# Performance work log

Measured on AMD Instinct MI355X. Metric: run time of the kernel, lower is better.

## Reference

```python
import jax, jax.numpy as jnp
import numpy as np

B, S, DM = 2, 2048, 1024
H, HD = 16, 64  # heads, head_dims = dims // heads
SCALE = HD ** -0.5


def softmax_one(x):
    # softmax with +1 in the denominator: exp(x_i) / (1 + sum_j exp(x_j))
    # stable form: shift by m = max(max(x), 0)
    m = jnp.maximum(jnp.max(x, axis=-1, keepdims=True), 0.0)
    e = jnp.exp(x - m)
    return e / (jnp.exp(-m) + jnp.sum(e, axis=-1, keepdims=True))


def setup_inputs() -> dict:
    key = jax.random.key(0)
    ks = jax.random.split(key, 11)
    init = lambda k, shape, fan_in: jax.random.uniform(k, shape, jnp.float32, -1.0, 1.0) * (fan_in ** -0.5)
    return {
        "query": jax.random.normal(ks[0], (B, S, DM), jnp.float32),
        "key": jax.random.normal(ks[1], (B, S, DM), jnp.float32),
        "value": jax.random.normal(ks[2], (B, S, DM), jnp.float32),
        "Wq": init(ks[3], (H * HD, DM), DM), "bq": init(ks[4], (H * HD,), DM),
        "Wk": init(ks[5], (H * HD, DM), DM), "bk": init(ks[6], (H * HD,), DM),
        "Wv": init(ks[7], (H * HD, DM), DM), "bv": init(ks[8], (H * HD,), DM),
        "Wo": init(ks[9], (DM, H * HD), H * HD), "bo": init(ks[10], (DM,), H * HD),
    }


def _proj(x, W, b):
    # [B,S,DM] -> [B,H,S,HD]
    y = x @ W.T + b
    return y.reshape(B, S, H, HD).transpose(0, 2, 1, 3)


def reference(query, key, value, Wq, bq, Wk, bk, Wv, bv, Wo, bo):
    Q = _proj(query, Wq, bq)
    K = _proj(key, Wk, bk)
    V = _proj(value, Wv, bv)
    scores = jnp.einsum("bhqd,bhkd->bhqk", Q, K) * SCALE  # [B,H,S,S]
    attn = softmax_one(scores)
    out = jnp.einsum("bhqk,bhkd->bhqd", attn, V)  # [B,H,S,HD]
    out = out.transpose(0, 2, 1, 3).reshape(B, S, H * HD)
    return out @ Wo.T + bo
```

## Files before the change

### kernel.cpp

```cpp
#include <hip/hip_runtime.h>

#define B_ 2
#define S_ 2048
#define DM_ 1024
#define H_ 16
#define HD_ 64
#define QSCALE_ 0.18033688011112042f

typedef __bf16 bf16;
typedef __attribute__((ext_vector_type(4))) __bf16 bf16x4;
typedef __attribute__((ext_vector_type(8))) __bf16 bf16x8;
typedef __attribute__((ext_vector_type(4))) float f32x4;

#define MFMA16(a, b, c) __builtin_amdgcn_mfma_f32_16x16x32_bf16((a), (b), (c), 0, 0, 0)
#define EXP2(x) __builtin_amdgcn_exp2f(x)

__device__ __forceinline__ void async16(const bf16* g, bf16* l) {
  __builtin_amdgcn_global_load_lds(
      (const __attribute__((address_space(1))) void*)g,
      (__attribute__((address_space(3))) void*)l, 16, 0, 0);
}

__global__ __launch_bounds__(256) void convert_kernel(
    const float* __restrict__ q, const float* __restrict__ k,
    const float* __restrict__ v, const float* __restrict__ wq,
    const float* __restrict__ wk, const float* __restrict__ wv,
    const float* __restrict__ wo, bf16* __restrict__ dst) {
  size_t idx = ((size_t)blockIdx.x * 256 + threadIdx.x) * 8;
  const float* src;
  size_t off;
  if (idx < 4194304) { src = q; off = idx; }
  else if (idx < 8388608) { src = k; off = idx - 4194304; }
  else if (idx < 12582912) { src = v; off = idx - 8388608; }
  else if (idx < 13631488) { src = wq; off = idx - 12582912; }
  else if (idx < 14680064) { src = wk; off = idx - 13631488; }
  else if (idx < 15728640) { src = wv; off = idx - 14680064; }
  else { src = wo; off = idx - 15728640; }
  float4 a = *(const float4*)(src + off);
  float4 b = *(const float4*)(src + off + 4);
  bf16x8 o;
  o[0] = (bf16)a.x; o[1] = (bf16)a.y; o[2] = (bf16)a.z; o[3] = (bf16)a.w;
  o[4] = (bf16)b.x; o[5] = (bf16)b.y; o[6] = (bf16)b.z; o[7] = (bf16)b.w;
  *(bf16x8*)(dst + idx) = o;
}

template <int MODE>
__device__ __forceinline__ void gemm_body(bf16* smem, const bf16* A,
                                          const bf16* W, const float* bias,
                                          bf16* C, float scale, int m0,
                                          int n0) {
  constexpr int K = 1024;
  bf16* As = smem;
  bf16* Bs = smem + 128 * 64;
  const int t = threadIdx.x;
  const int lane = t & 63, wave = t >> 6;
  const int quad = lane >> 4, l16 = lane & 15;
  const int wm = (wave >> 1) * 64, wn = (wave & 1) * 64;

  const f32x4 zero = {0.f, 0.f, 0.f, 0.f};
  f32x4 acc[4][4];
  for (int i = 0; i < 4; i++)
    for (int j = 0; j < 4; j++) acc[i][j] = zero;

  for (int k0 = 0; k0 < K; k0 += 64) {
    for (int i = 0; i < 4; ++i) {
      int c = i * 256 + t;
      int row = c >> 3, g = c & 7;
      int off = k0 + ((g ^ (row & 7)) * 8);
      async16(A + (size_t)(m0 + row) * K + off, As + c * 8);
      async16(W + (size_t)(n0 + row) * K + off, Bs + c * 8);
    }
    __syncthreads();

    for (int ks = 0; ks < 2; ks++) {
      bf16x8 af[4], bfr[4];
      for (int mb = 0; mb < 4; mb++) {
        int ra = wm + mb * 16 + l16;
        af[mb] = *(const bf16x8*)(As + ra * 64 + ((ks * 4 + quad) ^ (ra & 7)) * 8);
        int rb = wn + mb * 16 + l16;
        bfr[mb] = *(const bf16x8*)(Bs + rb * 64 + ((ks * 4 + quad) ^ (rb & 7)) * 8);
      }
      for (int mb = 0; mb < 4; mb++)
        for (int nb = 0; nb < 4; nb++)
          acc[mb][nb] = MFMA16(af[mb], bfr[nb], acc[mb][nb]);
    }
    __syncthreads();
  }

  if constexpr (MODE == 2) {
    bf16* Ct = smem;
    for (int nb = 0; nb < 4; nb++) {
      int cl = wn + nb * 16 + l16;
      float bv = bias[n0 + cl] * scale;
      for (int mb = 0; mb < 4; mb++) {
        int rowb = wm + mb * 16 + quad * 4;
        bf16x4 v;
        for (int r = 0; r < 4; r++)
          v[r] = (bf16)(acc[mb][nb][r] * scale + bv);
        *(bf16x4*)(Ct + cl * 136 + rowb) = v;
      }
    }
    __syncthreads();
    int c = t >> 1, half = t & 1;
    int colg = n0 + c;
    int hh = colg >> 6, dd = colg & 63;
    int bb = m0 >> 11, s0 = m0 & (S_ - 1);
    bf16* dst = C + (((size_t)(bb * H_ + hh)) * HD_ + dd) * S_ + s0 + half * 64;
    const bf16* srcr = Ct + c * 136 + half * 64;
    for (int j = 0; j < 8; ++j)
      *(bf16x8*)(dst + j * 8) = *(const bf16x8*)(srcr + j * 8);
  } else {
    for (int nb = 0; nb < 4; nb++) {
      int col = n0 + wn + nb * 16 + l16;
      float bv = bias[col] * scale;
      for (int mb = 0; mb < 4; mb++) {
        int rowb = m0 + wm + mb * 16 + quad * 4;
        for (int r = 0; r < 4; r++) {
          int row = rowb + r;
          float o = acc[mb][nb][r] * scale + bv;
          int bb = row >> 11, s = row & (S_ - 1);
          int h = col >> 6, d = col & 63;
          C[(((size_t)(bb * H_ + h)) * S_ + s) * HD_ + d] = (bf16)o;
        }
      }
    }
  }
}

__global__ __launch_bounds__(256, 4) void qkv_proj_kernel(
    const bf16* Xc, const float* bq, const float* bk, const float* bv,
    bf16* Qo, bf16* Ko, bf16* Vo) {
  __shared__ __align__(16) bf16 smem[128 * 136];
  int bid = blockIdx.x;
  int z = bid >> 8;
  int r = bid & 255;
  int c = r & 7;
  int j = r >> 3;
  int m0 = (c * 4 + (j & 3)) * 128;
  int n0 = (j >> 2) * 128;
  const bf16* A = Xc + (size_t)z * 4194304;
  const bf16* W = Xc + 12582912 + (size_t)z * 1048576;
  if (z == 0)
    gemm_body<1>(smem, A, W, bq, Qo, QSCALE_, m0, n0);
  else if (z == 1)
    gemm_body<1>(smem, A, W, bk, Ko, 1.0f, m0, n0);
  else
    gemm_body<2>(smem, A, W, bv, Vo, 1.0f, m0, n0);
}

__global__ __launch_bounds__(256, 4) void out_proj_kernel(const bf16* A,
                                                          const bf16* W,
                                                          const float* bias,
                                                          float* C) {
  constexpr int K = 1024, N = 1024;
  __shared__ __align__(16) bf16 As[64 * 64];
  __shared__ __align__(16) bf16 Bs[64 * 64];
  const int t = threadIdx.x;
  const int lane = t & 63, wave = t >> 6;
  const int quad = lane >> 4, l16 = lane & 15;
  int bid = blockIdx.x;
  int c = bid & 7;
  int j = bid >> 3;
  const int m0 = (c * 8 + (j & 7)) * 64;
  const int n0 = (j >> 3) * 64;

  const f32x4 zero = {0.f, 0.f, 0.f, 0.f};
  f32x4 acc[4];
  for (int i = 0; i < 4; i++) acc[i] = zero;

  for (int k0 = 0; k0 < K; k0 += 64) {
    for (int i = 0; i < 2; ++i) {
      int cc = i * 256 + t;
      int row = cc >> 3, g = cc & 7;
      int off = k0 + ((g ^ (row & 7)) * 8);
      async16(A + (size_t)(m0 + row) * K + off, As + cc * 8);
      async16(W + (size_t)(n0 + row) * K + off, Bs + cc * 8);
    }
    __syncthreads();

    for (int ks = 0; ks < 2; ks++) {
      int ra = wave * 16 + l16;
      bf16x8 af = *(const bf16x8*)(As + ra * 64 + ((ks * 4 + quad) ^ (ra & 7)) * 8);
      for (int nb = 0; nb < 4; nb++) {
        int rb = nb * 16 + l16;
        bf16x8 bfr =
            *(const bf16x8*)(Bs + rb * 64 + ((ks * 4 + quad) ^ (rb & 7)) * 8);
        acc[nb] = MFMA16(af, bfr, acc[nb]);
      }
    }
    __syncthreads();
  }

  for (int nb = 0; nb < 4; nb++) {
    int col = n0 + nb * 16 + l16;
    float bv = bias[col];
    int rowb = m0 + wave * 16 + quad * 4;
    for (int r = 0; r < 4; r++)
      C[(size_t)(rowb + r) * N + col] = acc[nb][r] + bv;
  }
}

__global__ __launch_bounds__(256, 2) void attn_kernel(
    const bf16* __restrict__ Q, const bf16* __restrict__ Kg,
    const bf16* __restrict__ VTg, bf16* __restrict__ O) {
  __shared__ __align__(16) bf16 Ks[128 * 64];
  __shared__ __align__(16) bf16 Vt[64 * 128];
  __shared__ __align__(16) bf16 Ps[4 * 64 * 72];
  __shared__ float rsL[2][64];
  const int t = threadIdx.x;
  const int lane = t & 63, wave = t >> 6;
  const int quad = lane >> 4, l16 = lane & 15;
  const int id = blockIdx.x;
  const int bh = id & 31;
  const int qt = id >> 5;
  const int q0 = qt * 128;
  const int b = bh >> 4, h = bh & 15;
  const int qhalf = wave >> 1, khalf = wave & 1;
  const size_t base = ((size_t)(b * H_ + h)) * S_ * HD_;
  const bf16* Qp = Q + base;
  const bf16* Kp = Kg + base;
  const bf16* Vp = VTg + base;

  bf16x8 aq[4][2];
  for (int s = 0; s < 4; s++) {
    const bf16* qr = Qp + (size_t)(q0 + qhalf * 64 + s * 16 + l16) * HD_;
    aq[s][0] = *(const bf16x8*)(qr + quad * 8);
    aq[s][1] = *(const bf16x8*)(qr + 32 + quad * 8);
  }

  const f32x4 zero = {0.f, 0.f, 0.f, 0.f};
  f32x4 oc[4][4];
  for (int s = 0; s < 4; s++)
    for (int d = 0; d < 4; d++) oc[s][d] = zero;
  float rs[4] = {0.f, 0.f, 0.f, 0.f};

  bf16* Pw = Ps + wave * (64 * 72);

  for (int kv0 = 0; kv0 < S_; kv0 += 128) {
    for (int i = 0; i < 4; ++i) {
      int c = i * 256 + t;
      int row = c >> 3, g = c & 7;
      async16(Kp + (size_t)(kv0 + row) * HD_ + (g ^ (row & 7)) * 8, Ks + c * 8);
    }
    for (int i = 0; i < 4; ++i) {
      int c = i * 256 + t;
      int d = c >> 4, g = c & 15;
      async16(Vp + (size_t)d * S_ + kv0 + (g ^ (d & 15)) * 8, Vt + c * 8);
    }
    __syncthreads();

    f32x4 sc[4][4];
    for (int s = 0; s < 4; s++)
      for (int nb = 0; nb < 4; nb++) sc[s][nb] = zero;
    for (int ks = 0; ks < 2; ks++) {
      for (int nb = 0; nb < 4; nb++) {
        int row = khalf * 64 + nb * 16 + l16;
        int slot = (ks * 4 + quad) ^ (row & 7);
        bf16x8 kf = *(const bf16x8*)(Ks + row * 64 + slot * 8);
        for (int s = 0; s < 4; s++)
          sc[s][nb] = MFMA16(kf, aq[s][ks], sc[s][nb]);
      }
    }

    for (int s = 0; s < 4; s++) {
      bf16* prow = Pw + (s * 16 + l16) * 72 + quad * 4;
      for (int nb = 0; nb < 4; nb++) {
        float p0 = EXP2(sc[s][nb][0]);
        float p1 = EXP2(sc[s][nb][1]);
        float p2 = EXP2(sc[s][nb][2]);
        float p3 = EXP2(sc[s][nb][3]);
        rs[s] += (p0 + p1) + (p2 + p3);
        bf16x4 pv = {(bf16)p0, (bf16)p1, (bf16)p2, (bf16)p3};
        *(bf16x4*)(prow + nb * 16) = pv;
      }
    }

    for (int ks2 = 0; ks2 < 2; ks2++) {
      bf16x8 vf[4];
      for (int db = 0; db < 4; db++) {
        int row = db * 16 + l16;
        int g = khalf * 8 + ks2 * 4 + quad;
        vf[db] = *(const bf16x8*)(Vt + row * 128 + (g ^ (row & 15)) * 8);
      }
      for (int s = 0; s < 4; s++) {
        bf16x8 ap =
            *(const bf16x8*)(Pw + (s * 16 + l16) * 72 + ks2 * 32 + quad * 8);
        for (int db = 0; db < 4; db++)
          oc[s][db] = MFMA16(ap, vf[db], oc[s][db]);
      }
    }
    __syncthreads();
  }

  float* Ld = (float*)Ps;
  if (khalf) {
    for (int s = 0; s < 4; s++) {
      float rtot = rs[s];
      rtot += __shfl_xor(rtot, 16);
      rtot += __shfl_xor(rtot, 32);
      if (quad == 0) rsL[qhalf][s * 16 + l16] = rtot;
      for (int db = 0; db < 4; db++)
        for (int r = 0; r < 4; r++)
          Ld[(size_t)qhalf * (64 * 68) + (s * 16 + quad * 4 + r) * 68 +
             db * 16 + l16] = oc[s][db][r];
    }
  }
  __syncthreads();
  if (!khalf) {
    for (int s = 0; s < 4; s++) {
      float rtot = rs[s];
      rtot += __shfl_xor(rtot, 16);
      rtot += __shfl_xor(rtot, 32);
      float l_all = 1.f + rtot + rsL[qhalf][s * 16 + l16];
      for (int r = 0; r < 4; r++) {
        float inv = 1.f / __shfl(l_all, quad * 4 + r);
        int qrow = q0 + qhalf * 64 + s * 16 + quad * 4 + r;
        size_t orow = ((size_t)(b * S_ + qrow) * H_ + h) * HD_;
        for (int db = 0; db < 4; db++) {
          float val = oc[s][db][r] +
                      Ld[(size_t)qhalf * (64 * 68) +
                         (s * 16 + quad * 4 + r) * 68 + db * 16 + l16];
          O[orow + db * 16 + l16] = (bf16)(val * inv);
        }
      }
    }
  }
}

extern "C" void kernel_launch(void* const* d_in, const int* in_sizes, int n_in,
                              void* d_out, int out_size, void* d_ws,
                              size_t ws_size, hipStream_t stream) {
  const float* query = (const float*)d_in[0];
  const float* key = (const float*)d_in[1];
  const float* value = (const float*)d_in[2];
  const float* bq = (const float*)d_in[4];
  const float* bk = (const float*)d_in[6];
  const float* bv = (const float*)d_in[8];
  const float* bo = (const float*)d_in[10];
  float* out = (float*)d_out;

  bf16* Xc = (bf16*)d_ws;
  bf16* Qw = Xc + 16777216;
  const size_t SZ = (size_t)B_ * H_ * S_ * HD_;
  bf16* Kw = Qw + SZ;
  bf16* Vw = Kw + SZ;
  bf16* Ow = Vw + SZ;

  convert_kernel<<<8192, 256, 0, stream>>>(query, key, value,
                                           (const float*)d_in[3],
                                           (const float*)d_in[5],
                                           (const float*)d_in[7],
                                           (const float*)d_in[9], Xc);
  qkv_proj_kernel<<<768, 256, 0, stream>>>(Xc, bq, bk, bv, Qw, Kw, Vw);
  attn_kernel<<<512, 256, 0, stream>>>(Qw, Kw, Vw, Ow);
  out_proj_kernel<<<1024, 256, 0, stream>>>(Ow, Xc + 15728640, bo, out);
}
```

Baseline: 206.1 us.

## Split attention KV tile across four waves with 64-row query tiles

The attention kernel now uses 512-thread blocks over 64-query tiles, so there are 1024 blocks instead of 512. Each of the 8 waves handles 32 query rows and one quarter of the 128-key tile, and the partial outputs and row sums are combined through a two-step LDS reduction. The goal is more parallelism and occupancy, with fewer registers per wave, to fill the GPU better. In exchange, each K/V tile is reloaded by twice as many blocks, per-wave MFMA work shrinks, and the epilogue adds an extra reduction pass and barrier.

After: 221.8 us. 7.6% more time.

```diff
diff --git a/kernel.cpp b/kernel.cpp
--- a/kernel.cpp
+++ b/kernel.cpp
@@ -200,71 +200,72 @@
   }
 }
 
-__global__ __launch_bounds__(256, 2) void attn_kernel(
+__global__ __launch_bounds__(512, 4) void attn_kernel(
     const bf16* __restrict__ Q, const bf16* __restrict__ Kg,
     const bf16* __restrict__ VTg, bf16* __restrict__ O) {
-  __shared__ __align__(16) bf16 Ks[128 * 64];
-  __shared__ __align__(16) bf16 Vt[64 * 128];
-  __shared__ __align__(16) bf16 Ps[4 * 64 * 72];
-  __shared__ float rsL[2][64];
+  __shared__ __align__(16) bf16 smem[26624];
   const int t = threadIdx.x;
   const int lane = t & 63, wave = t >> 6;
   const int quad = lane >> 4, l16 = lane & 15;
+  const int qh = wave >> 2;
+  const int kq = wave & 3;
   const int id = blockIdx.x;
   const int bh = id & 31;
   const int qt = id >> 5;
-  const int q0 = qt * 128;
+  const int q0 = qt * 64;
   const int b = bh >> 4, h = bh & 15;
-  const int qhalf = wave >> 1, khalf = wave & 1;
   const size_t base = ((size_t)(b * H_ + h)) * S_ * HD_;
   const bf16* Qp = Q + base;
   const bf16* Kp = Kg + base;
   const bf16* Vp = VTg + base;
 
-  bf16x8 aq[4][2];
-  for (int s = 0; s < 4; s++) {
-    const bf16* qr = Qp + (size_t)(q0 + qhalf * 64 + s * 16 + l16) * HD_;
+  bf16* Ks = smem;
+  bf16* Vt = smem + 8192;
+  bf16* Pw = smem + 16384 + wave * (32 * 40);
+
+  bf16x8 aq[2][2];
+  for (int s = 0; s < 2; s++) {
+    const bf16* qr = Qp + (size_t)(q0 + qh * 32 + s * 16 + l16) * HD_;
     aq[s][0] = *(const bf16x8*)(qr + quad * 8);
     aq[s][1] = *(const bf16x8*)(qr + 32 + quad * 8);
   }
 
   const f32x4 zero = {0.f, 0.f, 0.f, 0.f};
-  f32x4 oc[4][4];
-  for (int s = 0; s < 4; s++)
+  f32x4 oc[2][4];
+  for (int s = 0; s < 2; s++)
     for (int d = 0; d < 4; d++) oc[s][d] = zero;
-  float rs[4] = {0.f, 0.f, 0.f, 0.f};
-
-  bf16* Pw = Ps + wave * (64 * 72);
+  float rs[2] = {0.f, 0.f};
 
   for (int kv0 = 0; kv0 < S_; kv0 += 128) {
-    for (int i = 0; i < 4; ++i) {
-      int c = i * 256 + t;
-      int row = c >> 3, g = c & 7;
-      async16(Kp + (size_t)(kv0 + row) * HD_ + (g ^ (row & 7)) * 8, Ks + c * 8);
-    }
-    for (int i = 0; i < 4; ++i) {
-      int c = i * 256 + t;
-      int d = c >> 4, g = c & 15;
-      async16(Vp + (size_t)d * S_ + kv0 + (g ^ (d & 15)) * 8, Vt + c * 8);
-    }
-    __syncthreads();
-
-    f32x4 sc[4][4];
-    for (int s = 0; s < 4; s++)
-      for (int nb = 0; nb < 4; nb++) sc[s][nb] = zero;
+    for (int i = 0; i < 2; ++i) {
+      int cc = i * 512 + t;
+      int row = cc >> 3, g = cc & 7;
+      async16(Kp + (size_t)(kv0 + row) * HD_ + (g ^ (row & 7)) * 8,
+              Ks + cc * 8);
+    }
+    for (int i = 0; i < 2; ++i) {
+      int cc = i * 512 + t;
+      int d = cc >> 4, g = cc & 15;
+      async16(Vp + (size_t)d * S_ + kv0 + (g ^ (d & 15)) * 8, Vt + cc * 8);
+    }
+    __syncthreads();
+
+    f32x4 sc[2][2];
+    for (int s = 0; s < 2; s++)
+      for (int nb = 0; nb < 2; nb++) sc[s][nb] = zero;
     for (int ks = 0; ks < 2; ks++) {
-      for (int nb = 0; nb < 4; nb++) {
-        int row = khalf * 64 + nb * 16 + l16;
+      for (int nb = 0; nb < 2; nb++) {
+        int row = kq * 32 + nb * 16 + l16;
         int slot = (ks * 4 + quad) ^ (row & 7);
         bf16x8 kf = *(const bf16x8*)(Ks + row * 64 + slot * 8);
-        for (int s = 0; s < 4; s++)
+        for (int s = 0; s < 2; s++)
           sc[s][nb] = MFMA16(kf, aq[s][ks], sc[s][nb]);
       }
     }
 
-    for (int s = 0; s < 4; s++) {
-      bf16* prow = Pw + (s * 16 + l16) * 72 + quad * 4;
-      for (int nb = 0; nb < 4; nb++) {
+    for (int s = 0; s < 2; s++) {
+      bf16* prow = Pw + (s * 16 + l16) * 40 + quad * 4;
+      for (int nb = 0; nb < 2; nb++) {
         float p0 = EXP2(sc[s][nb][0]);
         float p1 = EXP2(sc[s][nb][1]);
         float p2 = EXP2(sc[s][nb][2]);
@@ -275,51 +276,72 @@
       }
     }
 
-    for (int ks2 = 0; ks2 < 2; ks2++) {
-      bf16x8 vf[4];
-      for (int db = 0; db < 4; db++) {
-        int row = db * 16 + l16;
-        int g = khalf * 8 + ks2 * 4 + quad;
-        vf[db] = *(const bf16x8*)(Vt + row * 128 + (g ^ (row & 15)) * 8);
-      }
-      for (int s = 0; s < 4; s++) {
-        bf16x8 ap =
-            *(const bf16x8*)(Pw + (s * 16 + l16) * 72 + ks2 * 32 + quad * 8);
-        for (int db = 0; db < 4; db++)
-          oc[s][db] = MFMA16(ap, vf[db], oc[s][db]);
-      }
-    }
-    __syncthreads();
-  }
-
-  float* Ld = (float*)Ps;
-  if (khalf) {
-    for (int s = 0; s < 4; s++) {
-      float rtot = rs[s];
-      rtot += __shfl_xor(rtot, 16);
-      rtot += __shfl_xor(rtot, 32);
-      if (quad == 0) rsL[qhalf][s * 16 + l16] = rtot;
+    bf16x8 vf[4];
+    for (int db = 0; db < 4; db++) {
+      int row = db * 16 + l16;
+      int g = kq * 4 + quad;
+      vf[db] = *(const bf16x8*)(Vt + row * 128 + (g ^ (row & 15)) * 8);
+    }
+    for (int s = 0; s < 2; s++) {
+      bf16x8 ap = *(const bf16x8*)(Pw + (s * 16 + l16) * 40 + quad * 8);
+      for (int db = 0; db < 4; db++)
+        oc[s][db] = MFMA16(ap, vf[db], oc[s][db]);
+    }
+
+    __syncthreads();
+  }
+
+  float rtot[2];
+  for (int s = 0; s < 2; s++) {
+    float v = rs[s];
+    v += __shfl_xor(v, 16);
+    v += __shfl_xor(v, 32);
+    rtot[s] = v;
+  }
+
+  float* Ld = (float*)smem;
+  float* rsL = (float*)(smem + 17408);
+
+  if (kq & 1) {
+    float* Lw = Ld + (size_t)((qh * 2 + (kq >> 1)) * 32) * 68;
+    for (int s = 0; s < 2; s++) {
       for (int db = 0; db < 4; db++)
         for (int r = 0; r < 4; r++)
-          Ld[(size_t)qhalf * (64 * 68) + (s * 16 + quad * 4 + r) * 68 +
-             db * 16 + l16] = oc[s][db][r];
+          Lw[(s * 16 + quad * 4 + r) * 68 + db * 16 + l16] = oc[s][db][r];
+      if (quad == 0) rsL[(qh * 2 + (kq >> 1)) * 32 + s * 16 + l16] = rtot[s];
     }
   }
   __syncthreads();
-  if (!khalf) {
-    for (int s = 0; s < 4; s++) {
-      float rtot = rs[s];
-      rtot += __shfl_xor(rtot, 16);
-      rtot += __shfl_xor(rtot, 32);
-      float l_all = 1.f + rtot + rsL[qhalf][s * 16 + l16];
+  if (!(kq & 1)) {
+    float* Lr = Ld + (size_t)((qh * 2 + (kq >> 1)) * 32) * 68;
+    for (int s = 0; s < 2; s++) {
+      for (int db = 0; db < 4; db++)
+        for (int r = 0; r < 4; r++)
+          oc[s][db][r] += Lr[(s * 16 + quad * 4 + r) * 68 + db * 16 + l16];
+      rtot[s] += rsL[(qh * 2 + (kq >> 1)) * 32 + s * 16 + l16];
+    }
+  }
+  if (kq == 2) {
+    float* Lw = Ld + (size_t)((qh * 2 + 1) * 32) * 68;
+    for (int s = 0; s < 2; s++) {
+      for (int db = 0; db < 4; db++)
+        for (int r = 0; r < 4; r++)
+          Lw[(s * 16 + quad * 4 + r) * 68 + db * 16 + l16] = oc[s][db][r];
+      if (quad == 0) rsL[(qh * 2 + 1) * 32 + s * 16 + l16] = rtot[s];
+    }
+  }
+  __syncthreads();
+  if (kq == 0) {
+    float* Lr = Ld + (size_t)((qh * 2 + 1) * 32) * 68;
+    for (int s = 0; s < 2; s++) {
+      float l_all = 1.f + rtot[s] + rsL[(qh * 2 + 1) * 32 + s * 16 + l16];
       for (int r = 0; r < 4; r++) {
         float inv = 1.f / __shfl(l_all, quad * 4 + r);
-        int qrow = q0 + qhalf * 64 + s * 16 + quad * 4 + r;
+        int qrow = q0 + qh * 32 + s * 16 + quad * 4 + r;
         size_t orow = ((size_t)(b * S_ + qrow) * H_ + h) * HD_;
         for (int db = 0; db < 4; db++) {
           float val = oc[s][db][r] +
-                      Ld[(size_t)qhalf * (64 * 68) +
-                         (s * 16 + quad * 4 + r) * 68 + db * 16 + l16];
+                      Lr[(s * 16 + quad * 4 + r) * 68 + db * 16 + l16];
           O[orow + db * 16 + l16] = (bf16)(val * inv);
         }
       }
@@ -352,6 +374,6 @@
                                            (const float*)d_in[7],
                                            (const float*)d_in[9], Xc);
   qkv_proj_kernel<<<768, 256, 0, stream>>>(Xc, bq, bk, bv, Qw, Kw, Vw);
-  attn_kernel<<<512, 256, 0, stream>>>(Qw, Kw, Vw, Ow);
+  attn_kernel<<<1024, 512, 0, stream>>>(Qw, Kw, Vw, Ow);
   out_proj_kernel<<<1024, 256, 0, stream>>>(Ow, Xc + 15728640, bo, out);
 }
```
